# Kernel optimization log

Measured on AMD Instinct MI355X. Metric: run time of the kernel, lower is better.

## Reference

```python
import jax, jax.numpy as jnp
import numpy as np

N, D, R, E, ED = 50000, 128, 8, 800000, 32
BN_EPS = 1e-5


def _bn(x, g, b):
    # training-mode BatchNorm1d: biased batch stats over axis 0
    m = jnp.mean(x, axis=0)
    v = jnp.var(x, axis=0)
    return (x - m) * jax.lax.rsqrt(v + BN_EPS) * g + b


def _aggregate(x, node_in, nor, ew_norm, edge_feature, We, be):
    # fused: ew * x[node_in] + ew * edge_linear(edge_feature), single scatter-add
    msg = ew_norm[:, None] * (x[node_in] + edge_feature @ We + be)  # [E, D]
    return jax.ops.segment_sum(msg, nor, num_segments=N * R)  # [N*R, D]


def _forward(x, node_in, node_out, relation, edge_weight, edge_feature,
             l1_Wlin, l1_blin, l1_Wself, l1_bself, l1_Wedge, l1_bedge, l1_g, l1_b,
             l2_Wlin, l2_blin, l2_Wself, l2_bself, l2_Wedge, l2_bedge, l2_g, l2_b):
    nor = node_out * R + relation  # [E], expanded destination index
    deg = jax.ops.segment_sum(edge_weight, nor, num_segments=N * R)
    ew = edge_weight / deg[nor]  # degree-normalized edge weights
    # layer 1: relationalGraphConv (update viewed as [N, R*D])
    u1 = _aggregate(x, node_in, nor, ew, edge_feature, l1_Wedge, l1_bedge)
    u1 = u1.reshape(N, R * D)
    h = u1 @ l1_Wlin + l1_blin + x @ l1_Wself + l1_bself
    h = jax.nn.relu(_bn(h, l1_g, l1_b))
    # layer 2: relationalGraph (update permuted to [R*N, D])
    u2 = _aggregate(h, node_in, nor, ew, edge_feature, l2_Wedge, l2_bedge)
    u2 = u2.reshape(N, R, D).transpose(1, 0, 2).reshape(R * N, D)
    h_rep = jnp.tile(h, (R, 1))  # input.repeat(num_relation, 1)
    o = u2 @ l2_Wlin + l2_blin + h_rep @ l2_Wself + l2_bself
    o = jax.nn.relu(_bn(o, l2_g, l2_b))
    return o.reshape(R, N, D)


def setup_inputs() -> dict:
    key = jax.random.key(0)
    ks = jax.random.split(key, 12)
    s_in = 1.0 / np.sqrt(D)
    s_lin1 = 1.0 / np.sqrt(R * D)
    s_e = 1.0 / np.sqrt(ED)
    return {
        "x": jax.random.normal(ks[0], (N, D), jnp.float32),
        "node_in": jax.random.randint(ks[1], (E,), 0, N),
        "node_out": jax.random.randint(ks[2], (E,), 0, N),
        "relation": jax.random.randint(ks[3], (E,), 0, R),
        "edge_weight": jnp.ones((E,), jnp.float32),
        "edge_feature": jax.random.normal(ks[4], (E, ED), jnp.float32),
        "l1_Wlin": jax.random.normal(ks[5], (R * D, D), jnp.float32) * s_lin1,
        "l1_blin": jnp.zeros((D,), jnp.float32),
        "l1_Wself": jax.random.normal(ks[6], (D, D), jnp.float32) * s_in,
        "l1_bself": jnp.zeros((D,), jnp.float32),
        "l1_Wedge": jax.random.normal(ks[7], (ED, D), jnp.float32) * s_e,
        "l1_bedge": jnp.zeros((D,), jnp.float32),
        "l1_g": jnp.ones((D,), jnp.float32),
        "l1_b": jnp.zeros((D,), jnp.float32),
        "l2_Wlin": jax.random.normal(ks[8], (D, D), jnp.float32) * s_in,
        "l2_blin": jnp.zeros((D,), jnp.float32),
        "l2_Wself": jax.random.normal(ks[9], (D, D), jnp.float32) * s_in,
        "l2_bself": jnp.zeros((D,), jnp.float32),
        "l2_Wedge": jax.random.normal(ks[10], (ED, D), jnp.float32) * s_e,
        "l2_bedge": jnp.zeros((D,), jnp.float32),
        "l2_g": jnp.ones((D,), jnp.float32),
        "l2_b": jnp.zeros((D,), jnp.float32),
    }


def reference(x, node_in, node_out, relation, edge_weight, edge_feature,
              l1_Wlin, l1_blin, l1_Wself, l1_bself, l1_Wedge, l1_bedge, l1_g, l1_b,
              l2_Wlin, l2_blin, l2_Wself, l2_bself, l2_Wedge, l2_bedge, l2_g, l2_b):
    return _forward(x, node_in, node_out, relation, edge_weight, edge_feature,
                    l1_Wlin, l1_blin, l1_Wself, l1_bself, l1_Wedge, l1_bedge, l1_g, l1_b,
                    l2_Wlin, l2_blin, l2_Wself, l2_bself, l2_Wedge, l2_bedge, l2_g, l2_b)
```

## Files before the change

### kernel.cpp

```cpp
#include <hip/hip_runtime.h>
#include <hip/hip_bf16.h>

#define Nn 50000
#define Dd 128
#define Rr 8
#define Ee 800000
#define EDd 32
#define NR (Nn * Rr)
#define BN_EPS 1e-5f
#define NREP 16

typedef __attribute__((ext_vector_type(8))) short short8;
typedef __attribute__((ext_vector_type(4))) float floatx4;
typedef unsigned short u16;

__device__ inline float bf2f(u16 u) {
    unsigned int x = ((unsigned int)u) << 16;
    return __uint_as_float(x);
}
__device__ inline u16 f2bf(float f) {
    __hip_bfloat16 h = __float2bfloat16(f);
    return *(u16*)&h;
}

__global__ __launch_bounds__(256) void k_deg(const int* __restrict__ node_out,
                                             const int* __restrict__ relation,
                                             const float* __restrict__ w_in,
                                             float* __restrict__ deg,
                                             int* __restrict__ cnt) {
    int e = blockIdx.x * 256 + threadIdx.x;
    if (e >= Ee) return;
    int idx = node_out[e] * Rr + relation[e];
    unsafeAtomicAdd(deg + idx, w_in[e]);
    atomicAdd(cnt + idx, 1);
}

__global__ __launch_bounds__(256) void k_scan1(const int* __restrict__ cnt,
                                               int* __restrict__ base,
                                               int* __restrict__ partials) {
    __shared__ int sd[256];
    int b0 = blockIdx.x * 1024;
    int t = threadIdx.x;
    int v[4], s = 0;
    #pragma unroll
    for (int j = 0; j < 4; ++j) {
        int idx = b0 + t * 4 + j;
        v[j] = (idx < NR) ? cnt[idx] : 0;
        s += v[j];
    }
    sd[t] = s;
    __syncthreads();
    for (int off = 1; off < 256; off <<= 1) {
        int xv = (t >= off) ? sd[t - off] : 0;
        __syncthreads();
        sd[t] += xv;
        __syncthreads();
    }
    int excl = sd[t] - s;
    if (t == 255) partials[blockIdx.x] = sd[255];
    int run = excl;
    #pragma unroll
    for (int j = 0; j < 4; ++j) {
        int idx = b0 + t * 4 + j;
        if (idx < NR) base[idx] = run;
        run += v[j];
    }
}

__global__ __launch_bounds__(512) void k_scan2(int* __restrict__ partials, int n) {
    __shared__ int sd[512];
    int t = threadIdx.x;
    int own = (t < n) ? partials[t] : 0;
    sd[t] = own;
    __syncthreads();
    for (int off = 1; off < 512; off <<= 1) {
        int xv = (t >= off) ? sd[t - off] : 0;
        __syncthreads();
        sd[t] += xv;
        __syncthreads();
    }
    if (t < n) partials[t] = sd[t] - own;
}

__global__ __launch_bounds__(256) void k_scan3(int* __restrict__ base,
                                               const int* __restrict__ partials) {
    int b0 = blockIdx.x * 1024;
    int add = partials[blockIdx.x];
    int t = threadIdx.x;
    #pragma unroll
    for (int j = 0; j < 4; ++j) {
        int idx = b0 + t * 4 + j;
        if (idx < NR) base[idx] += add;
    }
}

__global__ __launch_bounds__(256) void k_scatter(const int* __restrict__ node_in,
                                                 const int* __restrict__ node_out,
                                                 const int* __restrict__ relation,
                                                 const float* __restrict__ w_in,
                                                 const float* __restrict__ deg,
                                                 int* __restrict__ base,
                                                 int4* __restrict__ recs) {
    int e = blockIdx.x * 256 + threadIdx.x;
    if (e >= Ee) return;
    int idx = node_out[e] * Rr + relation[e];
    int pos = atomicAdd(base + idx, 1);
    int4 r;
    r.x = node_in[e];
    r.y = __float_as_int(w_in[e] / deg[idx]);
    r.z = e;
    r.w = 0;
    recs[pos] = r;
}

__global__ __launch_bounds__(256) void k_cvt(const float* __restrict__ src,
                                             u16* __restrict__ dst, long n) {
    long i = ((long)blockIdx.x * 256 + threadIdx.x) * 4;
    if (i >= n) return;
    float4 v = *(const float4*)(src + i);
    ushort4 o;
    o.x = f2bf(v.x); o.y = f2bf(v.y); o.z = f2bf(v.z); o.w = f2bf(v.w);
    *(ushort4*)(dst + i) = o;
}

__global__ __launch_bounds__(256) void k_prepB(const float* __restrict__ W1,
                                               const float* __restrict__ Ws1,
                                               const float* __restrict__ W2,
                                               const float* __restrict__ Ws2,
                                               u16* __restrict__ Bt) {
    int idx = blockIdx.x * 256 + threadIdx.x;
    if (idx >= 11 * 16384) return;
    int p = idx >> 14;
    int n = (idx >> 7) & 127;
    int k = idx & 127;
    float v;
    if (p < 8)       v = W1[((p << 7) + k) * 128 + n];
    else if (p == 8) v = Ws1[k * 128 + n];
    else if (p == 9) v = W2[k * 128 + n];
    else             v = Ws2[k * 128 + n];
    Bt[((long)p << 14) + n * 128 + k] = f2bf(v);
}

__global__ __launch_bounds__(256) void k_prepWef1(const float* __restrict__ We,
                                                  const float* __restrict__ be,
                                                  const float* __restrict__ Wlin,
                                                  u16* __restrict__ out) {
    int idx = blockIdx.x * 256 + threadIdx.x;
    if (idx >= 3 * 16384) return;
    int n = (idx >> 7) & 127;
    int k = idx & 127;
    int kk = (idx >> 14) * 128 + k;
    int p = kk / 40, j = kk % 40;
    float acc = 0.f;
    if (kk < 320 && j < 33) {
        for (int t = 0; t < 128; ++t) {
            float m = (j < 32) ? We[j * 128 + t] : be[t];
            acc = fmaf(m, Wlin[(p * 128 + t) * 128 + n], acc);
        }
    }
    out[idx] = f2bf(acc);
}

__global__ __launch_bounds__(256) void k_prepWef2(const float* __restrict__ We,
                                                  const float* __restrict__ be,
                                                  const float* __restrict__ Wlin,
                                                  u16* __restrict__ out) {
    int idx = blockIdx.x * 256 + threadIdx.x;
    if (idx >= 8192) return;
    int n = idx >> 6;
    int k = idx & 63;
    float acc = 0.f;
    if (k < 33) {
        for (int t = 0; t < 128; ++t) {
            float m = (k < 32) ? We[k * 128 + t] : be[t];
            acc = fmaf(m, Wlin[t * 128 + n], acc);
        }
    }
    out[idx] = f2bf(acc);
}

__global__ __launch_bounds__(256) void k_agg1(const u16* __restrict__ src,
                                              const int* __restrict__ base_end,
                                              const int* __restrict__ cnt,
                                              const int4* __restrict__ recs,
                                              const float* __restrict__ ef,
                                              u16* __restrict__ u,
                                              u16* __restrict__ aggef_x) {
    int gid = threadIdx.x >> 4;
    int gl = threadIdx.x & 15;
    int gl8 = gl * 8, gl2 = gl * 2;
    for (long d = (long)blockIdx.x * 16 + gid; d < NR; d += (long)gridDim.x * 16) {
        int end = base_end[d];
        int c = cnt[d];
        int e = end - c;
        float a[8] = {0.f, 0.f, 0.f, 0.f, 0.f, 0.f, 0.f, 0.f};
        float e0 = 0.f, e1 = 0.f;
        for (; e + 2 <= end; e += 2) {
            int4 r0 = recs[e];
            int4 r1 = recs[e + 1];
            short8 x0 = *(const short8*)(src + (long)r0.x * Dd + gl8);
            short8 x1 = *(const short8*)(src + (long)r1.x * Dd + gl8);
            float2 f0 = *(const float2*)(ef + (long)r0.z * EDd + gl2);
            float2 f1 = *(const float2*)(ef + (long)r1.z * EDd + gl2);
            float w0 = __int_as_float(r0.y);
            float w1 = __int_as_float(r1.y);
            #pragma unroll
            for (int j = 0; j < 8; ++j) {
                a[j] = fmaf(w0, bf2f((u16)x0[j]), a[j]);
                a[j] = fmaf(w1, bf2f((u16)x1[j]), a[j]);
            }
            e0 = fmaf(w0, f0.x, e0); e0 = fmaf(w1, f1.x, e0);
            e1 = fmaf(w0, f0.y, e1); e1 = fmaf(w1, f1.y, e1);
        }
        if (e < end) {
            int4 r0 = recs[e];
            float w0 = __int_as_float(r0.y);
            short8 x0 = *(const short8*)(src + (long)r0.x * Dd + gl8);
            float2 f0 = *(const float2*)(ef + (long)r0.z * EDd + gl2);
            #pragma unroll
            for (int j = 0; j < 8; ++j)
                a[j] = fmaf(w0, bf2f((u16)x0[j]), a[j]);
            e0 = fmaf(w0, f0.x, e0);
            e1 = fmaf(w0, f0.y, e1);
        }
        short8 o;
        #pragma unroll
        for (int j = 0; j < 8; ++j) o[j] = (short)f2bf(a[j]);
        *(short8*)(u + d * Dd + gl8) = o;
        ushort2 ev;
        ev.x = f2bf(e0);
        ev.y = f2bf(e1);
        *(ushort2*)(aggef_x + d * 40 + gl2) = ev;
        if (gl < 4) {
            ushort2 t;
            t.x = (gl == 0 && c > 0) ? (u16)0x3F80 : (u16)0;
            t.y = 0;
            *(ushort2*)(aggef_x + d * 40 + 32 + gl2) = t;
        }
    }
}

__global__ __launch_bounds__(256) void k_agg2(const u16* __restrict__ src,
                                              const int* __restrict__ base_end,
                                              const int* __restrict__ cnt,
                                              const int4* __restrict__ recs,
                                              u16* __restrict__ u) {
    int gid = threadIdx.x >> 4;
    int gl = threadIdx.x & 15;
    int gl8 = gl * 8;
    for (long d = (long)blockIdx.x * 16 + gid; d < NR; d += (long)gridDim.x * 16) {
        int end = base_end[d];
        int c = cnt[d];
        int e = end - c;
        float a[8] = {0.f, 0.f, 0.f, 0.f, 0.f, 0.f, 0.f, 0.f};
        for (; e + 2 <= end; e += 2) {
            int4 r0 = recs[e];
            int4 r1 = recs[e + 1];
            short8 x0 = *(const short8*)(src + (long)r0.x * Dd + gl8);
            short8 x1 = *(const short8*)(src + (long)r1.x * Dd + gl8);
            float w0 = __int_as_float(r0.y);
            float w1 = __int_as_float(r1.y);
            #pragma unroll
            for (int j = 0; j < 8; ++j) {
                a[j] = fmaf(w0, bf2f((u16)x0[j]), a[j]);
                a[j] = fmaf(w1, bf2f((u16)x1[j]), a[j]);
            }
        }
        if (e < end) {
            int4 r0 = recs[e];
            float w0 = __int_as_float(r0.y);
            short8 x0 = *(const short8*)(src + (long)r0.x * Dd + gl8);
            #pragma unroll
            for (int j = 0; j < 8; ++j)
                a[j] = fmaf(w0, bf2f((u16)x0[j]), a[j]);
        }
        short8 o;
        #pragma unroll
        for (int j = 0; j < 8; ++j) o[j] = (short)f2bf(a[j]);
        *(short8*)(u + d * Dd + gl8) = o;
    }
}

template <int NK>
__device__ __forceinline__ void l1_panel(const u16* __restrict__ Ap,
                                         const long* __restrict__ aoff,
                                         const u16* __restrict__ Bp, int br0, int br1,
                                         int kq8, floatx4 (&acc)[4][2]) {
    short8 a[4][NK], b[2][NK];
    #pragma unroll
    for (int kk = 0; kk < NK; ++kk) {
        #pragma unroll
        for (int ti = 0; ti < 4; ++ti)
            a[ti][kk] = *(const short8*)(Ap + aoff[ti] + kk * 32 + kq8);
        b[0][kk] = *(const short8*)(Bp + (long)br0 * 128 + kk * 32 + kq8);
        b[1][kk] = *(const short8*)(Bp + (long)br1 * 128 + kk * 32 + kq8);
    }
    #pragma unroll
    for (int kk = 0; kk < NK; ++kk)
        #pragma unroll
        for (int ti = 0; ti < 4; ++ti)
            #pragma unroll
            for (int tj = 0; tj < 2; ++tj)
                acc[ti][tj] = __builtin_amdgcn_mfma_f32_16x16x32_bf16(
                    a[ti][kk], b[tj][kk], acc[ti][tj], 0, 0, 0);
}

template <int NK>
__device__ __forceinline__ void l2_panel(const u16* __restrict__ Ap,
                                         const long* __restrict__ aoff,
                                         const u16* __restrict__ Bp, long bstride,
                                         const int* __restrict__ brow, int koff,
                                         int kq8, floatx4 (&acc)[4][4]) {
    short8 a[4][NK], b[4][NK];
    #pragma unroll
    for (int kk = 0; kk < NK; ++kk) {
        #pragma unroll
        for (int ti = 0; ti < 4; ++ti)
            a[ti][kk] = *(const short8*)(Ap + aoff[ti] + koff + kk * 32 + kq8);
        #pragma unroll
        for (int tj = 0; tj < 4; ++tj)
            b[tj][kk] = *(const short8*)(Bp + (long)brow[tj] * bstride + koff + kk * 32 + kq8);
    }
    #pragma unroll
    for (int kk = 0; kk < NK; ++kk)
        #pragma unroll
        for (int ti = 0; ti < 4; ++ti)
            #pragma unroll
            for (int tj = 0; tj < 4; ++tj)
                acc[ti][tj] = __builtin_amdgcn_mfma_f32_16x16x32_bf16(
                    a[ti][kk], b[tj][kk], acc[ti][tj], 0, 0, 0);
}

__global__ __launch_bounds__(256) void k_gemm_l1(const u16* __restrict__ U,
                                                 const u16* __restrict__ Xb,
                                                 const u16* __restrict__ Bt,
                                                 const u16* __restrict__ Wef,
                                                 const u16* __restrict__ Ax,
                                                 u16* __restrict__ Hpre,
                                                 float* __restrict__ stats) {
    const int tid = threadIdx.x;
    const int wave = tid >> 6, lane = tid & 63;
    const int l15 = lane & 15, kq = lane >> 4;
    const int kq8 = kq * 8;
    const int n0w = wave * 32;
    const int m0 = blockIdx.x * 64;
    const int br0 = n0w + l15, br1 = n0w + 16 + l15;

    floatx4 acc[4][2];
    #pragma unroll
    for (int i = 0; i < 4; ++i)
        #pragma unroll
        for (int j = 0; j < 2; ++j)
            acc[i][j] = (floatx4){0.f, 0.f, 0.f, 0.f};

    long mb[4];
    int mrow[4];
    #pragma unroll
    for (int ti = 0; ti < 4; ++ti) {
        int m = m0 + ti * 16 + l15;
        if (m >= Nn) m = Nn - 1;
        mrow[ti] = m;
        mb[ti] = (long)m * 1024;
    }

    long aoff[4];
    #pragma unroll
    for (int p = 0; p < 8; ++p) {
        #pragma unroll
        for (int ti = 0; ti < 4; ++ti) aoff[ti] = mb[ti] + p * 128;
        l1_panel<4>(U, aoff, Bt + ((long)p << 14), br0, br1, kq8, acc);
    }
    #pragma unroll
    for (int ti = 0; ti < 4; ++ti) aoff[ti] = (long)mrow[ti] * 128;
    l1_panel<4>(Xb, aoff, Bt + (8L << 14), br0, br1, kq8, acc);
    #pragma unroll
    for (int q = 0; q < 2; ++q) {
        #pragma unroll
        for (int ti = 0; ti < 4; ++ti) aoff[ti] = (long)mrow[ti] * 320 + q * 128;
        l1_panel<4>(Ax, aoff, Wef + ((long)q << 14), br0, br1, kq8, acc);
    }
    #pragma unroll
    for (int ti = 0; ti < 4; ++ti) aoff[ti] = (long)mrow[ti] * 320 + 256;
    l1_panel<2>(Ax, aoff, Wef + (2L << 14), br0, br1, kq8, acc);

    float cs[2] = {0.f, 0.f}, cq[2] = {0.f, 0.f};
    #pragma unroll
    for (int ti = 0; ti < 4; ++ti) {
        #pragma unroll
        for (int r = 0; r < 4; ++r) {
            int m = m0 + ti * 16 + kq * 4 + r;
            if (m < Nn) {
                #pragma unroll
                for (int tj = 0; tj < 2; ++tj) {
                    float v = acc[ti][tj][r];
                    int col = n0w + tj * 16 + l15;
                    Hpre[(long)m * Dd + col] = f2bf(v);
                    cs[tj] += v;
                    cq[tj] = fmaf(v, v, cq[tj]);
                }
            }
        }
    }
    #pragma unroll
    for (int tj = 0; tj < 2; ++tj) {
        cs[tj] += __shfl_xor(cs[tj], 16, 64);
        cs[tj] += __shfl_xor(cs[tj], 32, 64);
        cq[tj] += __shfl_xor(cq[tj], 16, 64);
        cq[tj] += __shfl_xor(cq[tj], 32, 64);
    }
    if (kq == 0) {
        int rep = blockIdx.x & (NREP - 1);
        #pragma unroll
        for (int tj = 0; tj < 2; ++tj) {
            int col = n0w + tj * 16 + l15;
            unsafeAtomicAdd(stats + rep * 256 + col, cs[tj]);
            unsafeAtomicAdd(stats + rep * 256 + 128 + col, cq[tj]);
        }
    }
}

__global__ __launch_bounds__(256) void k_gemm_l2(const u16* __restrict__ U,
                                                 const u16* __restrict__ H,
                                                 const u16* __restrict__ Bt2,
                                                 const u16* __restrict__ Wef2,
                                                 const u16* __restrict__ Ax,
                                                 float* __restrict__ Out,
                                                 float* __restrict__ stats) {
    const int tid = threadIdx.x;
    const int wave = tid >> 6, lane = tid & 63;
    const int l15 = lane & 15, kq = lane >> 4;
    const int kq8 = kq * 8;
    const int wm = wave & 1, wn = wave >> 1;
    const int n0w = wn * 64;
    const long m0 = (long)blockIdx.x * 128;

    int brow[4];
    #pragma unroll
    for (int tj = 0; tj < 4; ++tj) brow[tj] = n0w + tj * 16 + l15;

    floatx4 acc[4][4];
    #pragma unroll
    for (int i = 0; i < 4; ++i)
        #pragma unroll
        for (int j = 0; j < 4; ++j)
            acc[i][j] = (floatx4){0.f, 0.f, 0.f, 0.f};

    long aoffU[4], aoffH[4], aoffE[4];
    #pragma unroll
    for (int ti = 0; ti < 4; ++ti) {
        long mm = m0 + wm * 64 + ti * 16 + l15;
        int n = (int)(mm % Nn);
        int r = (int)(mm / Nn);
        long dd = (long)n * 8 + r;
        aoffU[ti] = dd * 128;
        aoffH[ti] = (long)n * 128;
        aoffE[ti] = dd * 40;
    }

    l2_panel<2>(U, aoffU, Bt2, 128, brow, 0, kq8, acc);
    l2_panel<2>(U, aoffU, Bt2, 128, brow, 64, kq8, acc);
    l2_panel<2>(H, aoffH, Bt2 + 16384, 128, brow, 0, kq8, acc);
    l2_panel<2>(H, aoffH, Bt2 + 16384, 128, brow, 64, kq8, acc);
    l2_panel<2>(Ax, aoffE, Wef2, 64, brow, 0, kq8, acc);

    float cs[4] = {0.f, 0.f, 0.f, 0.f}, cq[4] = {0.f, 0.f, 0.f, 0.f};
    #pragma unroll
    for (int ti = 0; ti < 4; ++ti) {
        #pragma unroll
        for (int r = 0; r < 4; ++r) {
            long mm = m0 + wm * 64 + ti * 16 + kq * 4 + r;
            #pragma unroll
            for (int tj = 0; tj < 4; ++tj) {
                float v = acc[ti][tj][r];
                int col = n0w + tj * 16 + l15;
                Out[mm * Dd + col] = v;
                cs[tj] += v;
                cq[tj] = fmaf(v, v, cq[tj]);
            }
        }
    }
    #pragma unroll
    for (int tj = 0; tj < 4; ++tj) {
        cs[tj] += __shfl_xor(cs[tj], 16, 64);
        cs[tj] += __shfl_xor(cs[tj], 32, 64);
        cq[tj] += __shfl_xor(cq[tj], 16, 64);
        cq[tj] += __shfl_xor(cq[tj], 32, 64);
    }
    if (kq == 0) {
        int rep = blockIdx.x & (NREP - 1);
        #pragma unroll
        for (int tj = 0; tj < 4; ++tj) {
            int col = n0w + tj * 16 + l15;
            unsafeAtomicAdd(stats + rep * 256 + col, cs[tj]);
            unsafeAtomicAdd(stats + rep * 256 + 128 + col, cq[tj]);
        }
    }
}

__global__ __launch_bounds__(256) void k_bn_apply_bf(u16* __restrict__ X,
                                                     const float* __restrict__ stats,
                                                     const float* __restrict__ g,
                                                     const float* __restrict__ b, int M) {
    int c = (threadIdx.x & 31) * 4;
    int rh = threadIdx.x >> 5;
    float invM = 1.0f / (float)M;
    float s[4] = {0, 0, 0, 0}, q[4] = {0, 0, 0, 0};
    for (int rep = 0; rep < NREP; ++rep) {
        float4 s4 = *(const float4*)(stats + rep * 256 + c);
        float4 q4 = *(const float4*)(stats + rep * 256 + 128 + c);
        s[0] += s4.x; s[1] += s4.y; s[2] += s4.z; s[3] += s4.w;
        q[0] += q4.x; q[1] += q4.y; q[2] += q4.z; q[3] += q4.w;
    }
    float4 g4 = *(const float4*)(g + c);
    float4 b4 = *(const float4*)(b + c);
    float gv[4] = {g4.x, g4.y, g4.z, g4.w};
    float bv[4] = {b4.x, b4.y, b4.z, b4.w};
    float sc[4], sh[4];
    #pragma unroll
    for (int j = 0; j < 4; ++j) {
        float m = s[j] * invM;
        sc[j] = gv[j] / sqrtf(q[j] * invM - m * m + BN_EPS);
        sh[j] = bv[j] - m * sc[j];
    }
    for (long r = blockIdx.x * 8 + rh; r < M; r += (long)gridDim.x * 8) {
        ushort4 v = *(ushort4*)(X + r * Dd + c);
        ushort4 o;
        o.x = f2bf(fmaxf(fmaf(bf2f(v.x), sc[0], sh[0]), 0.f));
        o.y = f2bf(fmaxf(fmaf(bf2f(v.y), sc[1], sh[1]), 0.f));
        o.z = f2bf(fmaxf(fmaf(bf2f(v.z), sc[2], sh[2]), 0.f));
        o.w = f2bf(fmaxf(fmaf(bf2f(v.w), sc[3], sh[3]), 0.f));
        *(ushort4*)(X + r * Dd + c) = o;
    }
}

__global__ __launch_bounds__(256) void k_bn_apply_f32(float* __restrict__ X,
                                                      const float* __restrict__ stats,
                                                      const float* __restrict__ g,
                                                      const float* __restrict__ b, int M) {
    int c = (threadIdx.x & 31) * 4;
    int rh = threadIdx.x >> 5;
    float invM = 1.0f / (float)M;
    float s[4] = {0, 0, 0, 0}, q[4] = {0, 0, 0, 0};
    for (int rep = 0; rep < NREP; ++rep) {
        float4 s4 = *(const float4*)(stats + rep * 256 + c);
        float4 q4 = *(const float4*)(stats + rep * 256 + 128 + c);
        s[0] += s4.x; s[1] += s4.y; s[2] += s4.z; s[3] += s4.w;
        q[0] += q4.x; q[1] += q4.y; q[2] += q4.z; q[3] += q4.w;
    }
    float4 g4 = *(const float4*)(g + c);
    float4 b4 = *(const float4*)(b + c);
    float gv[4] = {g4.x, g4.y, g4.z, g4.w};
    float bv[4] = {b4.x, b4.y, b4.z, b4.w};
    float sc[4], sh[4];
    #pragma unroll
    for (int j = 0; j < 4; ++j) {
        float m = s[j] * invM;
        sc[j] = gv[j] / sqrtf(q[j] * invM - m * m + BN_EPS);
        sh[j] = bv[j] - m * sc[j];
    }
    for (long r = blockIdx.x * 8 + rh; r < M; r += (long)gridDim.x * 8) {
        float4 v = *(float4*)(X + r * Dd + c);
        v.x = fmaxf(fmaf(v.x, sc[0], sh[0]), 0.f);
        v.y = fmaxf(fmaf(v.y, sc[1], sh[1]), 0.f);
        v.z = fmaxf(fmaf(v.z, sc[2], sh[2]), 0.f);
        v.w = fmaxf(fmaf(v.w, sc[3], sh[3]), 0.f);
        *(float4*)(X + r * Dd + c) = v;
    }
}

extern "C" void kernel_launch(void* const* d_in, const int* in_sizes, int n_in,
                              void* d_out, int out_size, void* d_ws, size_t ws_size,
                              hipStream_t stream) {
    const float* x            = (const float*)d_in[0];
    const int*   node_in      = (const int*)d_in[1];
    const int*   node_out     = (const int*)d_in[2];
    const int*   relation     = (const int*)d_in[3];
    const float* edge_weight  = (const float*)d_in[4];
    const float* edge_feature = (const float*)d_in[5];
    const float* l1_Wlin  = (const float*)d_in[6];
    const float* l1_Wself = (const float*)d_in[8];
    const float* l1_Wedge = (const float*)d_in[10];
    const float* l1_bedge = (const float*)d_in[11];
    const float* l1_g     = (const float*)d_in[12];
    const float* l1_b     = (const float*)d_in[13];
    const float* l2_Wlin  = (const float*)d_in[14];
    const float* l2_Wself = (const float*)d_in[16];
    const float* l2_Wedge = (const float*)d_in[18];
    const float* l2_bedge = (const float*)d_in[19];
    const float* l2_g     = (const float*)d_in[20];
    const float* l2_b     = (const float*)d_in[21];
    float* out = (float*)d_out;

    u16* u_bf    = (u16*)d_ws;
    u16* h       = u_bf + (long)NR * Dd;
    u16* x_bf    = h + (long)Nn * Dd;
    u16* aggef_x = x_bf + (long)Nn * Dd;
    u16* Bt      = aggef_x + (long)NR * 40 + 128;
    u16* Wef1    = Bt + 11 * 16384;
    u16* Wef2    = Wef1 + 3 * 16384;
    float* deg   = (float*)(Wef2 + 8192);
    int*   cnt   = (int*)(deg + NR);
    int*   base  = cnt + NR;
    int4*  recs  = (int4*)(base + NR);
    int*   partials = (int*)(recs + Ee);
    float* stats = (float*)(partials + 1024);

    const int NB1 = (NR + 1023) / 1024;

    hipMemsetAsync(deg, 0, sizeof(float) * NR, stream);
    hipMemsetAsync(cnt, 0, sizeof(int) * NR, stream);
    hipMemsetAsync(stats, 0, sizeof(float) * 2 * NREP * 256, stream);
    hipMemsetAsync(aggef_x + (long)NR * 40, 0, 256, stream);
    k_deg<<<(Ee + 255) / 256, 256, 0, stream>>>(node_out, relation, edge_weight, deg, cnt);
    k_scan1<<<NB1, 256, 0, stream>>>(cnt, base, partials);
    k_scan2<<<1, 512, 0, stream>>>(partials, NB1);
    k_scan3<<<NB1, 256, 0, stream>>>(base, partials);
    k_scatter<<<(Ee + 255) / 256, 256, 0, stream>>>(node_in, node_out, relation, edge_weight,
                                                    deg, base, recs);
    k_cvt<<<((long)Nn * Dd / 4 + 255) / 256, 256, 0, stream>>>(x, x_bf, (long)Nn * Dd);
    k_prepB<<<(11 * 16384 + 255) / 256, 256, 0, stream>>>(l1_Wlin, l1_Wself, l2_Wlin, l2_Wself, Bt);
    k_prepWef1<<<(3 * 16384 + 255) / 256, 256, 0, stream>>>(l1_Wedge, l1_bedge, l1_Wlin, Wef1);
    k_prepWef2<<<32, 256, 0, stream>>>(l2_Wedge, l2_bedge, l2_Wlin, Wef2);

    k_agg1<<<4096, 256, 0, stream>>>(x_bf, base, cnt, recs, edge_feature, u_bf, aggef_x);
    k_gemm_l1<<<(Nn + 63) / 64, 256, 0, stream>>>(u_bf, x_bf, Bt, Wef1, aggef_x, h, stats);
    k_bn_apply_bf<<<512, 256, 0, stream>>>(h, stats, l1_g, l1_b, Nn);

    k_agg2<<<4096, 256, 0, stream>>>(h, base, cnt, recs, u_bf);
    k_gemm_l2<<<NR / 128, 256, 0, stream>>>(u_bf, h, Bt + 9 * 16384, Wef2, aggef_x, out,
                                            stats + NREP * 256);
    k_bn_apply_f32<<<2048, 256, 0, stream>>>(out, stats + NREP * 256, l2_g, l2_b, NR);
}
```

Baseline: 928.5 us.

## Reassociate layer-2 GEMM before aggregation and fuse BN statistics into gather

Layer 2 now multiplies h by Wlin and Wself once per node (N rows instead of N*R) and gathers the pre-transformed rows. The bias and edge-feature terms are added through a separate small GEMM. The gather kernel also accumulates the BatchNorm sums, and the final kernel applies the norm while transposing into the output layout. Intermediates are stored as fp16 instead of fp32, which cuts traffic but adds rounding error. Layer-1 aggregation is unrolled by four edges to expose more memory parallelism.

```diff
diff --git a/kernel.cpp b/kernel.cpp
--- a/kernel.cpp
+++ b/kernel.cpp
@@ -21,6 +21,14 @@
 __device__ inline u16 f2bf(float f) {
     __hip_bfloat16 h = __float2bfloat16(f);
     return *(u16*)&h;
+}
+__device__ inline u16 f2h(float f) {
+    _Float16 h = (_Float16)f;
+    return *(u16*)&h;
+}
+__device__ inline float h2f(u16 u) {
+    _Float16 h = *(_Float16*)&u;
+    return (float)h;
 }
 
 __global__ __launch_bounds__(256) void k_deg(const int* __restrict__ node_out,
@@ -195,15 +203,38 @@
         int e = end - c;
         float a[8] = {0.f, 0.f, 0.f, 0.f, 0.f, 0.f, 0.f, 0.f};
         float e0 = 0.f, e1 = 0.f;
-        for (; e + 2 <= end; e += 2) {
-            int4 r0 = recs[e];
-            int4 r1 = recs[e + 1];
+        for (; e + 4 <= end; e += 4) {
+            int4 r0 = recs[e],     r1 = recs[e + 1];
+            int4 r2 = recs[e + 2], r3 = recs[e + 3];
+            short8 x0 = *(const short8*)(src + (long)r0.x * Dd + gl8);
+            short8 x1 = *(const short8*)(src + (long)r1.x * Dd + gl8);
+            short8 x2 = *(const short8*)(src + (long)r2.x * Dd + gl8);
+            short8 x3 = *(const short8*)(src + (long)r3.x * Dd + gl8);
+            float2 f0 = *(const float2*)(ef + (long)r0.z * EDd + gl2);
+            float2 f1 = *(const float2*)(ef + (long)r1.z * EDd + gl2);
+            float2 f2 = *(const float2*)(ef + (long)r2.z * EDd + gl2);
+            float2 f3 = *(const float2*)(ef + (long)r3.z * EDd + gl2);
+            float w0 = __int_as_float(r0.y), w1 = __int_as_float(r1.y);
+            float w2 = __int_as_float(r2.y), w3 = __int_as_float(r3.y);
+            #pragma unroll
+            for (int j = 0; j < 8; ++j) {
+                a[j] = fmaf(w0, bf2f((u16)x0[j]), a[j]);
+                a[j] = fmaf(w1, bf2f((u16)x1[j]), a[j]);
+                a[j] = fmaf(w2, bf2f((u16)x2[j]), a[j]);
+                a[j] = fmaf(w3, bf2f((u16)x3[j]), a[j]);
+            }
+            e0 = fmaf(w0, f0.x, e0); e0 = fmaf(w1, f1.x, e0);
+            e0 = fmaf(w2, f2.x, e0); e0 = fmaf(w3, f3.x, e0);
+            e1 = fmaf(w0, f0.y, e1); e1 = fmaf(w1, f1.y, e1);
+            e1 = fmaf(w2, f2.y, e1); e1 = fmaf(w3, f3.y, e1);
+        }
+        if (e + 2 <= end) {
+            int4 r0 = recs[e], r1 = recs[e + 1];
             short8 x0 = *(const short8*)(src + (long)r0.x * Dd + gl8);
             short8 x1 = *(const short8*)(src + (long)r1.x * Dd + gl8);
             float2 f0 = *(const float2*)(ef + (long)r0.z * EDd + gl2);
             float2 f1 = *(const float2*)(ef + (long)r1.z * EDd + gl2);
-            float w0 = __int_as_float(r0.y);
-            float w1 = __int_as_float(r1.y);
+            float w0 = __int_as_float(r0.y), w1 = __int_as_float(r1.y);
             #pragma unroll
             for (int j = 0; j < 8; ++j) {
                 a[j] = fmaf(w0, bf2f((u16)x0[j]), a[j]);
@@ -211,6 +242,7 @@
             }
             e0 = fmaf(w0, f0.x, e0); e0 = fmaf(w1, f1.x, e0);
             e1 = fmaf(w0, f0.y, e1); e1 = fmaf(w1, f1.y, e1);
+            e += 2;
         }
         if (e < end) {
             int4 r0 = recs[e];
@@ -237,47 +269,6 @@
             t.y = 0;
             *(ushort2*)(aggef_x + d * 40 + 32 + gl2) = t;
         }
-    }
-}
-
-__global__ __launch_bounds__(256) void k_agg2(const u16* __restrict__ src,
-                                              const int* __restrict__ base_end,
-                                              const int* __restrict__ cnt,
-                                              const int4* __restrict__ recs,
-                                              u16* __restrict__ u) {
-    int gid = threadIdx.x >> 4;
-    int gl = threadIdx.x & 15;
-    int gl8 = gl * 8;
-    for (long d = (long)blockIdx.x * 16 + gid; d < NR; d += (long)gridDim.x * 16) {
-        int end = base_end[d];
-        int c = cnt[d];
-        int e = end - c;
-        float a[8] = {0.f, 0.f, 0.f, 0.f, 0.f, 0.f, 0.f, 0.f};
-        for (; e + 2 <= end; e += 2) {
-            int4 r0 = recs[e];
-            int4 r1 = recs[e + 1];
-            short8 x0 = *(const short8*)(src + (long)r0.x * Dd + gl8);
-            short8 x1 = *(const short8*)(src + (long)r1.x * Dd + gl8);
-            float w0 = __int_as_float(r0.y);
-            float w1 = __int_as_float(r1.y);
-            #pragma unroll
-            for (int j = 0; j < 8; ++j) {
-                a[j] = fmaf(w0, bf2f((u16)x0[j]), a[j]);
-                a[j] = fmaf(w1, bf2f((u16)x1[j]), a[j]);
-            }
-        }
-        if (e < end) {
-            int4 r0 = recs[e];
-            float w0 = __int_as_float(r0.y);
-            short8 x0 = *(const short8*)(src + (long)r0.x * Dd + gl8);
-            #pragma unroll
-            for (int j = 0; j < 8; ++j)
-                a[j] = fmaf(w0, bf2f((u16)x0[j]), a[j]);
-        }
-        short8 o;
-        #pragma unroll
-        for (int j = 0; j < 8; ++j) o[j] = (short)f2bf(a[j]);
-        *(short8*)(u + d * Dd + gl8) = o;
     }
 }
 
@@ -419,13 +410,54 @@
     }
 }
 
-__global__ __launch_bounds__(256) void k_gemm_l2(const u16* __restrict__ U,
-                                                 const u16* __restrict__ H,
-                                                 const u16* __restrict__ Bt2,
-                                                 const u16* __restrict__ Wef2,
-                                                 const u16* __restrict__ Ax,
-                                                 float* __restrict__ Out,
-                                                 float* __restrict__ stats) {
+__global__ __launch_bounds__(256) void k_gemm_ht(const u16* __restrict__ H,
+                                                 const u16* __restrict__ Bt,
+                                                 u16* __restrict__ ht,
+                                                 u16* __restrict__ hsp) {
+    const int tid = threadIdx.x;
+    const int wave = tid >> 6, lane = tid & 63;
+    const int l15 = lane & 15, kq = lane >> 4;
+    const int kq8 = kq * 8;
+    const int n0w = wave * 32;
+    const int m0 = blockIdx.x * 64;
+    const int br0 = n0w + l15, br1 = n0w + 16 + l15;
+
+    long aoff[4];
+    #pragma unroll
+    for (int ti = 0; ti < 4; ++ti) {
+        int m = m0 + ti * 16 + l15;
+        if (m >= Nn) m = Nn - 1;
+        aoff[ti] = (long)m * 128;
+    }
+
+    #pragma unroll
+    for (int which = 0; which < 2; ++which) {
+        floatx4 acc[4][2];
+        #pragma unroll
+        for (int i = 0; i < 4; ++i)
+            #pragma unroll
+            for (int j = 0; j < 2; ++j)
+                acc[i][j] = (floatx4){0.f, 0.f, 0.f, 0.f};
+        l1_panel<4>(H, aoff, Bt + ((long)(9 + which) << 14), br0, br1, kq8, acc);
+        u16* dst = which ? hsp : ht;
+        #pragma unroll
+        for (int ti = 0; ti < 4; ++ti) {
+            #pragma unroll
+            for (int r = 0; r < 4; ++r) {
+                int m = m0 + ti * 16 + kq * 4 + r;
+                if (m < Nn) {
+                    #pragma unroll
+                    for (int tj = 0; tj < 2; ++tj)
+                        dst[(long)m * Dd + n0w + tj * 16 + l15] = f2bf(acc[ti][tj][r]);
+                }
+            }
+        }
+    }
+}
+
+__global__ __launch_bounds__(256) void k_gemm_agf2(const u16* __restrict__ Ax,
+                                                   const u16* __restrict__ Wef2,
+                                                   u16* __restrict__ agf2) {
     const int tid = threadIdx.x;
     const int wave = tid >> 6, lane = tid & 63;
     const int l15 = lane & 15, kq = lane >> 4;
@@ -445,56 +477,105 @@
         for (int j = 0; j < 4; ++j)
             acc[i][j] = (floatx4){0.f, 0.f, 0.f, 0.f};
 
-    long aoffU[4], aoffH[4], aoffE[4];
-    #pragma unroll
-    for (int ti = 0; ti < 4; ++ti) {
-        long mm = m0 + wm * 64 + ti * 16 + l15;
-        int n = (int)(mm % Nn);
-        int r = (int)(mm / Nn);
-        long dd = (long)n * 8 + r;
-        aoffU[ti] = dd * 128;
-        aoffH[ti] = (long)n * 128;
-        aoffE[ti] = dd * 40;
-    }
-
-    l2_panel<2>(U, aoffU, Bt2, 128, brow, 0, kq8, acc);
-    l2_panel<2>(U, aoffU, Bt2, 128, brow, 64, kq8, acc);
-    l2_panel<2>(H, aoffH, Bt2 + 16384, 128, brow, 0, kq8, acc);
-    l2_panel<2>(H, aoffH, Bt2 + 16384, 128, brow, 64, kq8, acc);
+    long aoffE[4];
+    #pragma unroll
+    for (int ti = 0; ti < 4; ++ti)
+        aoffE[ti] = (m0 + wm * 64 + ti * 16 + l15) * 40L;
+
     l2_panel<2>(Ax, aoffE, Wef2, 64, brow, 0, kq8, acc);
 
-    float cs[4] = {0.f, 0.f, 0.f, 0.f}, cq[4] = {0.f, 0.f, 0.f, 0.f};
     #pragma unroll
     for (int ti = 0; ti < 4; ++ti) {
         #pragma unroll
         for (int r = 0; r < 4; ++r) {
             long mm = m0 + wm * 64 + ti * 16 + kq * 4 + r;
             #pragma unroll
-            for (int tj = 0; tj < 4; ++tj) {
-                float v = acc[ti][tj][r];
-                int col = n0w + tj * 16 + l15;
-                Out[mm * Dd + col] = v;
-                cs[tj] += v;
-                cq[tj] = fmaf(v, v, cq[tj]);
+            for (int tj = 0; tj < 4; ++tj)
+                agf2[mm * Dd + n0w + tj * 16 + l15] = f2h(acc[ti][tj][r]);
+        }
+    }
+}
+
+__global__ __launch_bounds__(256) void k_out(const u16* __restrict__ ht,
+                                             const u16* __restrict__ hsp,
+                                             const int* __restrict__ base_end,
+                                             const int* __restrict__ cnt,
+                                             const int4* __restrict__ recs,
+                                             u16* __restrict__ pre,
+                                             float* __restrict__ stats) {
+    __shared__ float sd[16][256];
+    int gid = threadIdx.x >> 4;
+    int gl = threadIdx.x & 15;
+    int gl8 = gl * 8;
+    float s[8] = {0, 0, 0, 0, 0, 0, 0, 0}, q[8] = {0, 0, 0, 0, 0, 0, 0, 0};
+    for (long d = (long)blockIdx.x * 16 + gid; d < NR; d += (long)gridDim.x * 16) {
+        int end = base_end[d];
+        int c = cnt[d];
+        int e = end - c;
+        long n = d >> 3;
+        short8 hv = *(const short8*)(hsp + n * Dd + gl8);
+        short8 gv = *(const short8*)(pre + d * Dd + gl8);
+        float a[8];
+        #pragma unroll
+        for (int j = 0; j < 8; ++j)
+            a[j] = bf2f((u16)hv[j]) + h2f((u16)gv[j]);
+        for (; e + 4 <= end; e += 4) {
+            int4 r0 = recs[e],     r1 = recs[e + 1];
+            int4 r2 = recs[e + 2], r3 = recs[e + 3];
+            short8 x0 = *(const short8*)(ht + (long)r0.x * Dd + gl8);
+            short8 x1 = *(const short8*)(ht + (long)r1.x * Dd + gl8);
+            short8 x2 = *(const short8*)(ht + (long)r2.x * Dd + gl8);
+            short8 x3 = *(const short8*)(ht + (long)r3.x * Dd + gl8);
+            float w0 = __int_as_float(r0.y), w1 = __int_as_float(r1.y);
+            float w2 = __int_as_float(r2.y), w3 = __int_as_float(r3.y);
+            #pragma unroll
+            for (int j = 0; j < 8; ++j) {
+                a[j] = fmaf(w0, bf2f((u16)x0[j]), a[j]);
+                a[j] = fmaf(w1, bf2f((u16)x1[j]), a[j]);
+                a[j] = fmaf(w2, bf2f((u16)x2[j]), a[j]);
+                a[j] = fmaf(w3, bf2f((u16)x3[j]), a[j]);
             }
         }
-    }
-    #pragma unroll
-    for (int tj = 0; tj < 4; ++tj) {
-        cs[tj] += __shfl_xor(cs[tj], 16, 64);
-        cs[tj] += __shfl_xor(cs[tj], 32, 64);
-        cq[tj] += __shfl_xor(cq[tj], 16, 64);
-        cq[tj] += __shfl_xor(cq[tj], 32, 64);
-    }
-    if (kq == 0) {
-        int rep = blockIdx.x & (NREP - 1);
-        #pragma unroll
-        for (int tj = 0; tj < 4; ++tj) {
-            int col = n0w + tj * 16 + l15;
-            unsafeAtomicAdd(stats + rep * 256 + col, cs[tj]);
-            unsafeAtomicAdd(stats + rep * 256 + 128 + col, cq[tj]);
-        }
-    }
+        if (e + 2 <= end) {
+            int4 r0 = recs[e], r1 = recs[e + 1];
+            short8 x0 = *(const short8*)(ht + (long)r0.x * Dd + gl8);
+            short8 x1 = *(const short8*)(ht + (long)r1.x * Dd + gl8);
+            float w0 = __int_as_float(r0.y), w1 = __int_as_float(r1.y);
+            #pragma unroll
+            for (int j = 0; j < 8; ++j) {
+                a[j] = fmaf(w0, bf2f((u16)x0[j]), a[j]);
+                a[j] = fmaf(w1, bf2f((u16)x1[j]), a[j]);
+            }
+            e += 2;
+        }
+        if (e < end) {
+            int4 r0 = recs[e];
+            float w0 = __int_as_float(r0.y);
+            short8 x0 = *(const short8*)(ht + (long)r0.x * Dd + gl8);
+            #pragma unroll
+            for (int j = 0; j < 8; ++j)
+                a[j] = fmaf(w0, bf2f((u16)x0[j]), a[j]);
+        }
+        short8 o;
+        #pragma unroll
+        for (int j = 0; j < 8; ++j) {
+            o[j] = (short)f2h(a[j]);
+            s[j] += a[j];
+            q[j] = fmaf(a[j], a[j], q[j]);
+        }
+        *(short8*)(pre + d * Dd + gl8) = o;
+    }
+    #pragma unroll
+    for (int j = 0; j < 8; ++j) {
+        sd[gid][gl8 + j] = s[j];
+        sd[gid][128 + gl8 + j] = q[j];
+    }
+    __syncthreads();
+    int t = threadIdx.x;
+    float acc = 0.f;
+    #pragma unroll
+    for (int g = 0; g < 16; ++g) acc += sd[g][t];
+    unsafeAtomicAdd(stats + (blockIdx.x & (NREP - 1)) * 256 + t, acc);
 }
 
 __global__ __launch_bounds__(256) void k_bn_apply_bf(u16* __restrict__ X,
@@ -533,13 +614,14 @@
     }
 }
 
-__global__ __launch_bounds__(256) void k_bn_apply_f32(float* __restrict__ X,
-                                                      const float* __restrict__ stats,
-                                                      const float* __restrict__ g,
-                                                      const float* __restrict__ b, int M) {
+__global__ __launch_bounds__(256) void k_bn_out(const u16* __restrict__ pre,
+                                                const float* __restrict__ stats,
+                                                const float* __restrict__ g,
+                                                const float* __restrict__ b,
+                                                float* __restrict__ out) {
     int c = (threadIdx.x & 31) * 4;
     int rh = threadIdx.x >> 5;
-    float invM = 1.0f / (float)M;
+    const float invM = 1.0f / (float)NR;
     float s[4] = {0, 0, 0, 0}, q[4] = {0, 0, 0, 0};
     for (int rep = 0; rep < NREP; ++rep) {
         float4 s4 = *(const float4*)(stats + rep * 256 + c);
@@ -558,13 +640,16 @@
         sc[j] = gv[j] / sqrtf(q[j] * invM - m * m + BN_EPS);
         sh[j] = bv[j] - m * sc[j];
     }
-    for (long r = blockIdx.x * 8 + rh; r < M; r += (long)gridDim.x * 8) {
-        float4 v = *(float4*)(X + r * Dd + c);
-        v.x = fmaxf(fmaf(v.x, sc[0], sh[0]), 0.f);
-        v.y = fmaxf(fmaf(v.y, sc[1], sh[1]), 0.f);
-        v.z = fmaxf(fmaf(v.z, sc[2], sh[2]), 0.f);
-        v.w = fmaxf(fmaf(v.w, sc[3], sh[3]), 0.f);
-        *(float4*)(X + r * Dd + c) = v;
+    for (int m = blockIdx.x * 8 + rh; m < NR; m += gridDim.x * 8) {
+        int r = m / Nn;
+        int n = m - r * Nn;
+        ushort4 v = *(const ushort4*)(pre + ((long)n * 8 + r) * Dd + c);
+        float4 o;
+        o.x = fmaxf(fmaf(h2f(v.x), sc[0], sh[0]), 0.f);
+        o.y = fmaxf(fmaf(h2f(v.y), sc[1], sh[1]), 0.f);
+        o.z = fmaxf(fmaf(h2f(v.z), sc[2], sh[2]), 0.f);
+        o.w = fmaxf(fmaf(h2f(v.w), sc[3], sh[3]), 0.f);
+        *(float4*)(out + (long)m * Dd + c) = o;
     }
 }
 
@@ -604,6 +689,9 @@
     int4*  recs  = (int4*)(base + NR);
     int*   partials = (int*)(recs + Ee);
     float* stats = (float*)(partials + 1024);
+    u16* agf2 = u_bf;
+    u16* ht   = x_bf;
+    u16* hsp  = aggef_x;
 
     const int NB1 = (NR + 1023) / 1024;
 
@@ -626,8 +714,8 @@
     k_gemm_l1<<<(Nn + 63) / 64, 256, 0, stream>>>(u_bf, x_bf, Bt, Wef1, aggef_x, h, stats);
     k_bn_apply_bf<<<512, 256, 0, stream>>>(h, stats, l1_g, l1_b, Nn);
 
-    k_agg2<<<4096, 256, 0, stream>>>(h, base, cnt, recs, u_bf);
-    k_gemm_l2<<<NR / 128, 256, 0, stream>>>(u_bf, h, Bt + 9 * 16384, Wef2, aggef_x, out,
-                                            stats + NREP * 256);
-    k_bn_apply_f32<<<2048, 256, 0, stream>>>(out, stats + NREP * 256, l2_g, l2_b, NR);
-}
+    k_gemm_agf2<<<NR / 128, 256, 0, stream>>>(aggef_x, Wef2, agf2);
+    k_gemm_ht<<<(Nn + 63) / 64, 256, 0, stream>>>(h, Bt, ht, hsp);
+    k_out<<<2048, 256, 0, stream>>>(ht, hsp, base, cnt, recs, agf2, stats + NREP * 256);
+    k_bn_out<<<2048, 256, 0, stream>>>(agf2, stats + NREP * 256, l2_g, l2_b, out);
+}
```

Result: faster. 866.0 us (-6.7%).
